# Performance work log

Measured on AMD Instinct MI355X. Metric: run time of the kernel, lower is better.

Reference implementation:

```python
import jax, jax.numpy as jnp
import numpy as np
import math

B, W, V, D, H, L = 64, 255, 16389, 512, 8, 8
S = W + 1          # window + cls token
NLOC = V - 5       # n_locations
CLS = V - 1        # cls_index = 16388
DH = D // H
FF = 4 * D


def _pe(seq_len, d):
    # Faithful to the quirky PositionalEmbedding: for even col c, sin(pos/10000**(2c/d));
    # for odd col c (= i+1), cos(pos/10000**(2c/d)) since it uses 2*(i+1)/d.
    pos = np.arange(seq_len, dtype=np.float32)[:, None]
    c = np.arange(d, dtype=np.float32)[None, :]
    ang = pos / (10000.0 ** (2.0 * c / d))
    pe = np.where(np.arange(d)[None, :] % 2 == 0, np.sin(ang), np.cos(ang))
    return jnp.asarray(pe, jnp.float32)

PE = _pe(S, D)


def _ln(x, s, b):
    m = x.mean(-1, keepdims=True)
    v = ((x - m) ** 2).mean(-1, keepdims=True)
    return (x - m) * jax.lax.rsqrt(v + 1e-5) * s + b


def setup_inputs() -> dict:
    key = jax.random.key(0)
    ks = jax.random.split(key, 8)
    sd = 0.02
    return {
        "x": jax.random.randint(ks[0], (B, W), 0, NLOC),
        "emb": jax.random.normal(ks[1], (V, D), jnp.float32) * sd,
        "qkv_w": jax.random.normal(ks[2], (L, D, 3 * D), jnp.float32) * sd,
        "qkv_b": jnp.zeros((L, 3 * D), jnp.float32),
        "out_w": jax.random.normal(ks[3], (L, D, D), jnp.float32) * sd,
        "out_b": jnp.zeros((L, D), jnp.float32),
        "ln1_s": jnp.ones((L, D), jnp.float32),
        "ln1_b": jnp.zeros((L, D), jnp.float32),
        "ln2_s": jnp.ones((L, D), jnp.float32),
        "ln2_b": jnp.zeros((L, D), jnp.float32),
        "ff1_w": jax.random.normal(ks[4], (L, D, FF), jnp.float32) * sd,
        "ff1_b": jnp.zeros((L, FF), jnp.float32),
        "ff2_w": jax.random.normal(ks[5], (L, FF, D), jnp.float32) * sd,
        "ff2_b": jnp.zeros((L, D), jnp.float32),
        "fn_s": jnp.ones((D,), jnp.float32),
        "fn_b": jnp.zeros((D,), jnp.float32),
        "head_w": jax.random.normal(ks[6], (D, V), jnp.float32) * sd,
    }


def _forward(x, emb, qkv_w, qkv_b, out_w, out_b, ln1_s, ln1_b, ln2_s, ln2_b,
             ff1_w, ff1_b, ff2_w, ff2_b, fn_s, fn_b, head_w):
    b = x.shape[0]
    xc = jnp.concatenate([x, jnp.full((b, 1), CLS, x.dtype)], axis=1)  # [B,S]
    h = emb[xc] + PE[None, :, :]

    def layer(h, p):
        qw, qb, ow, ob, l1s, l1b, l2s, l2b, w1, b1, w2, b2 = p
        x2 = _ln(h, l1s, l1b)
        qkv = x2 @ qw + qb                       # [B,S,3D]
        q, k, v = jnp.split(qkv, 3, axis=-1)
        sh = lambda t: t.reshape(b, S, H, DH).transpose(0, 2, 1, 3)  # [B,H,S,DH]
        q, k, v = sh(q), sh(k), sh(v)
        scores = jnp.einsum('bhqd,bhkd->bhqk', q, k) / math.sqrt(DH)
        attn = jax.nn.softmax(scores, axis=-1)
        o = jnp.einsum('bhqk,bhkd->bhqd', attn, v)
        o = o.transpose(0, 2, 1, 3).reshape(b, S, D)
        h = h + (o @ ow + ob)
        x2 = _ln(h, l2s, l2b)
        h = h + (jax.nn.relu(x2 @ w1 + b1) @ w2 + b2)
        return h, None

    h, _ = jax.lax.scan(layer, h, (qkv_w, qkv_b, out_w, out_b, ln1_s, ln1_b,
                                   ln2_s, ln2_b, ff1_w, ff1_b, ff2_w, ff2_b))
    h = _ln(h, fn_s, fn_b)
    # original projects every position then slices [:, -1, :NLOC]; projecting
    # only the last position with the first NLOC columns is identical math.
    return h[:, -1, :] @ head_w[:, :NLOC]        # [B, NLOC]


def reference(x, emb, qkv_w, qkv_b, out_w, out_b, ln1_s, ln1_b, ln2_s, ln2_b,
              ff1_w, ff1_b, ff2_w, ff2_b, fn_s, fn_b, head_w):
    return _forward(x, emb, qkv_w, qkv_b, out_w, out_b, ln1_s, ln1_b, ln2_s,
                    ln2_b, ff1_w, ff1_b, ff2_w, ff2_b, fn_s, fn_b, head_w)
```

## Files before the change

kernel.cpp:

```cpp
#include <hip/hip_runtime.h>
#include <hip/hip_bf16.h>
#include <math.h>

#define B_    64
#define W_    255
#define S_    256
#define V_    16389
#define NLOC_ 16384
#define CLS_  16388
#define D_    512
#define H_    8
#define DH_   64
#define FF_   2048
#define L_    8
#define NTOK  (B_ * S_)

typedef __attribute__((ext_vector_type(4)))  float f32x4;
typedef __attribute__((ext_vector_type(16))) float f32x16;
typedef __attribute__((ext_vector_type(8)))  short s16x8;

__device__ inline unsigned short f2b(float f) {
  union { float f; unsigned u; } v; v.f = f;
  unsigned r = v.u + 0x7fff + ((v.u >> 16) & 1);
  return (unsigned short)(r >> 16);
}
__device__ inline void gl_lds16(const void* g, void* l) {
  __builtin_amdgcn_global_load_lds((const __attribute__((address_space(1))) unsigned int*)g,
                                   (__attribute__((address_space(3))) unsigned int*)l, 16, 0, 0);
}
__device__ inline size_t tiled_off(int row, int k, int Kb) {
  return ((size_t)(row >> 7) * Kb + (k >> 5)) * 4096 +
         ((((k >> 3) & 3) * 128 + (row & 127)) * 8) + (k & 7);
}

__global__ __launch_bounds__(256) void embed_kernel(const int* __restrict__ x,
                                                    const float* __restrict__ emb,
                                                    float* __restrict__ h) {
  const int tok = blockIdx.x;
  const int bb = tok >> 8, ss = tok & 255;
  const int idx = (ss < W_) ? x[bb * W_ + ss] : CLS_;
  const float* e = emb + (size_t)idx * D_;
  float* hp = h + (size_t)tok * D_;
  #pragma unroll
  for (int r = 0; r < 2; ++r) {
    int d = threadIdx.x + r * 256;
    float ex = exp2f(-(float)d * (13.287712379549449f / 256.0f));
    float ang = (float)ss * ex;
    float pe = (d & 1) ? cosf(ang) : sinf(ang);
    hp[d] = e[d] + pe;
  }
}

template<bool TILED>
__global__ __launch_bounds__(256) void ln_kernel(const float* __restrict__ in,
                                                 unsigned short* __restrict__ out,
                                                 const float* __restrict__ sc,
                                                 const float* __restrict__ bi) {
  const int wave = threadIdx.x >> 6;
  const int tok = blockIdx.x * 4 + wave;
  const int lane = threadIdx.x & 63;
  const float* xp = in + (size_t)tok * D_;
  float4 a = *(const float4*)(xp + lane * 4);
  float4 b = *(const float4*)(xp + 256 + lane * 4);
  float sum = a.x + a.y + a.z + a.w + b.x + b.y + b.z + b.w;
  #pragma unroll
  for (int off = 32; off; off >>= 1) sum += __shfl_xor(sum, off);
  const float mean = sum * (1.0f / D_);
  float d0 = a.x - mean, d1 = a.y - mean, d2 = a.z - mean, d3 = a.w - mean;
  float e0 = b.x - mean, e1 = b.y - mean, e2 = b.z - mean, e3 = b.w - mean;
  float ss = d0*d0 + d1*d1 + d2*d2 + d3*d3 + e0*e0 + e1*e1 + e2*e2 + e3*e3;
  #pragma unroll
  for (int off = 32; off; off >>= 1) ss += __shfl_xor(ss, off);
  const float inv = rsqrtf(ss * (1.0f / D_) + 1e-5f);
  float4 s0 = *(const float4*)(sc + lane * 4);
  float4 s1 = *(const float4*)(sc + 256 + lane * 4);
  float4 b0 = *(const float4*)(bi + lane * 4);
  float4 b1 = *(const float4*)(bi + 256 + lane * 4);
  unsigned short o[8];
  o[0] = f2b(d0 * inv * s0.x + b0.x); o[1] = f2b(d1 * inv * s0.y + b0.y);
  o[2] = f2b(d2 * inv * s0.z + b0.z); o[3] = f2b(d3 * inv * s0.w + b0.w);
  o[4] = f2b(e0 * inv * s1.x + b1.x); o[5] = f2b(e1 * inv * s1.y + b1.y);
  o[6] = f2b(e2 * inv * s1.z + b1.z); o[7] = f2b(e3 * inv * s1.w + b1.w);
  if (!TILED) {
    unsigned short* yp = out + (size_t)tok * D_;
    *(ushort4*)(yp + lane * 4)       = *(const ushort4*)&o[0];
    *(ushort4*)(yp + 256 + lane * 4) = *(const ushort4*)&o[4];
  } else {
    __shared__ unsigned short Xs[4][512];
    *(ushort4*)&Xs[wave][lane * 4]       = *(const ushort4*)&o[0];
    *(ushort4*)&Xs[wave][256 + lane * 4] = *(const ushort4*)&o[4];
    __syncthreads();
    const int c = threadIdx.x >> 2, tr = threadIdx.x & 3;
    const int tok0 = blockIdx.x * 4;
    const int rb = tok0 >> 7, r = (tok0 & 127) + tr;
    s16x8 v = *(const s16x8*)&Xs[tr][c * 8];
    *(s16x8*)(out + ((size_t)rb * 16 + (c >> 2)) * 4096 + ((c & 3) * 128 + r) * 8) = v;
  }
}

__global__ __launch_bounds__(256) void wconv_kernel(const float* __restrict__ W,
                                                    unsigned short* __restrict__ Wt,
                                                    int ldn, int Kb,
                                                    long in_stride, long out_stride) {
  const float* Wl = W + (size_t)blockIdx.z * in_stride;
  unsigned short* Wo = Wt + (size_t)blockIdx.z * out_stride +
                       ((size_t)blockIdx.x * Kb + blockIdx.y) * 4096;
  const int k0 = blockIdx.y * 32, n0 = blockIdx.x * 128;
  #pragma unroll
  for (int qq = 0; qq < 2; ++qq) {
    int q = qq * 256 + threadIdx.x;
    int c = q >> 7, r = q & 127;
    unsigned short o[8];
    #pragma unroll
    for (int j = 0; j < 8; ++j)
      o[j] = f2b(Wl[(size_t)(k0 + c * 8 + j) * ldn + n0 + r]);
    *(s16x8*)(Wo + (size_t)q * 8) = *(const s16x8*)o;
  }
}

template<bool BIAS, bool RELU, bool RES, bool OUTBF, bool ATILED, bool OUTTILED>
__global__ __launch_bounds__(256) void mfma_gemm(
    const unsigned short* __restrict__ A, long lda,
    const unsigned short* __restrict__ Bt,
    const float* __restrict__ bias,
    float* __restrict__ Cres,
    unsigned short* __restrict__ Cbf,
    int M, int N, int K, int ldc, int kbo) {
  __shared__ __align__(16) unsigned char smem[16384];
  unsigned short* As = (unsigned short*)smem;
  unsigned short* Bs = As + 128 * 32;
  const int tid = threadIdx.x;
  const int w = tid >> 6, lane = tid & 63;
  const int wm = w >> 1, wn = w & 1;
  int bx, by;
  {
    int nx = gridDim.x, ny = gridDim.y;
    int id = blockIdx.y * nx + blockIdx.x;
    if ((ny & 7) == 0) {
      int xcd = id & 7, k = id >> 3, band = ny >> 3;
      int kr = k / nx;
      by = xcd * band + kr;
      bx = k - kr * nx;
    } else { bx = blockIdx.x; by = blockIdx.y; }
  }
  const int row0 = by * 128, col0 = bx * 128;
  const int KbB = K >> 5;
  f32x16 acc[2][2] = {};
  const int fl = lane & 31, fg2 = lane >> 5;
  const int sc8 = w * 8;
  for (int k0 = 0; k0 < K; k0 += 32) {
    if (ATILED) {
      const unsigned short* at = A + ((size_t)(row0 >> 7) * lda + (k0 >> 5)) * 4096;
      gl_lds16(at + (size_t)tid * 8, As + (size_t)tid * 8);
      gl_lds16(at + (size_t)(256 + tid) * 8, As + (size_t)(256 + tid) * 8);
    } else {
      #pragma unroll
      for (int i = 0; i < 2; ++i) {
        int r = i * 64 + lane;
        int ar = row0 + r; if (ar >= M) ar = M - 1;
        gl_lds16(A + (size_t)ar * lda + k0 + sc8, As + (w * 2 + i) * 512);
      }
    }
    {
      const unsigned short* bt = Bt + ((size_t)(col0 >> 7) * KbB + (k0 >> 5)) * 4096;
      gl_lds16(bt + (size_t)tid * 8, Bs + (size_t)tid * 8);
      gl_lds16(bt + (size_t)(256 + tid) * 8, Bs + (size_t)(256 + tid) * 8);
    }
    __syncthreads();
    #pragma unroll
    for (int ks = 0; ks < 2; ++ks) {
      s16x8 af[2], bf2[2];
      #pragma unroll
      for (int mi = 0; mi < 2; ++mi)
        af[mi] = *(const s16x8*)&As[((ks * 2 + fg2) * 128 + wm * 64 + mi * 32 + fl) * 8];
      #pragma unroll
      for (int ni = 0; ni < 2; ++ni)
        bf2[ni] = *(const s16x8*)&Bs[((ks * 2 + fg2) * 128 + wn * 64 + ni * 32 + fl) * 8];
      #pragma unroll
      for (int mi = 0; mi < 2; ++mi)
        #pragma unroll
        for (int ni = 0; ni < 2; ++ni)
          acc[mi][ni] = __builtin_amdgcn_mfma_f32_32x32x16_bf16(af[mi], bf2[ni], acc[mi][ni], 0, 0, 0);
    }
    __syncthreads();
  }
  if (OUTTILED) {
    unsigned short* Cs = (unsigned short*)smem;
    #pragma unroll
    for (int half = 0; half < 2; ++half) {
      __syncthreads();
      if (wm == half) {
        #pragma unroll
        for (int mi = 0; mi < 2; ++mi)
          #pragma unroll
          for (int ni = 0; ni < 2; ++ni) {
            int col = wn * 64 + ni * 32 + fl;
            float bv = BIAS ? bias[col0 + col] : 0.0f;
            #pragma unroll
            for (int rg = 0; rg < 16; ++rg) {
              int rl = mi * 32 + (rg & 3) + 8 * (rg >> 2) + 4 * fg2;
              float v = acc[mi][ni][rg] + bv;
              if (RELU) v = fmaxf(v, 0.0f);
              Cs[((col >> 3) * 64 + rl) * 8 + (col & 7)] = f2b(v);
            }
          }
      }
      __syncthreads();
      #pragma unroll
      for (int i = 0; i < 4; ++i) {
        int vt = i * 256 + tid;
        int c = vt >> 6, r = vt & 63;
        int cg = (col0 >> 3) + c;
        s16x8 v = *(const s16x8*)&Cs[(size_t)vt * 8];
        *(s16x8*)(Cbf + ((size_t)(row0 >> 7) * kbo + (cg >> 2)) * 4096 +
                  ((cg & 3) * 128 + half * 64 + r) * 8) = v;
      }
    }
  } else if (OUTBF) {
    unsigned short* Cs = (unsigned short*)smem;
    #pragma unroll
    for (int half = 0; half < 2; ++half) {
      __syncthreads();
      if (wm == half) {
        #pragma unroll
        for (int mi = 0; mi < 2; ++mi)
          #pragma unroll
          for (int ni = 0; ni < 2; ++ni) {
            int col = wn * 64 + ni * 32 + fl;
            float bv = BIAS ? bias[col0 + col] : 0.0f;
            #pragma unroll
            for (int rg = 0; rg < 16; ++rg) {
              int rl = mi * 32 + (rg & 3) + 8 * (rg >> 2) + 4 * fg2;
              float v = acc[mi][ni][rg] + bv;
              if (RELU) v = fmaxf(v, 0.0f);
              Cs[rl * 128 + col] = f2b(v);
            }
          }
      }
      __syncthreads();
      #pragma unroll
      for (int i = 0; i < 4; ++i) {
        int chunk = i * 256 + tid;
        int row = chunk >> 4, cc = chunk & 15;
        int grow = row0 + half * 64 + row;
        *(s16x8*)(Cbf + (size_t)grow * ldc + col0 + cc * 8) =
            *(const s16x8*)&Cs[row * 128 + cc * 8];
      }
    }
  } else {
    float* Csf = (float*)smem;
    #pragma unroll
    for (int q = 0; q < 4; ++q) {
      __syncthreads();
      if (wm == (q >> 1)) {
        const int mi = q & 1;
        #pragma unroll
        for (int ni = 0; ni < 2; ++ni) {
          int col = wn * 64 + ni * 32 + fl;
          float bv = BIAS ? bias[col0 + col] : 0.0f;
          #pragma unroll
          for (int rg = 0; rg < 16; ++rg) {
            int rl = (rg & 3) + 8 * (rg >> 2) + 4 * fg2;
            float v = acc[mi][ni][rg] + bv;
            if (RELU) v = fmaxf(v, 0.0f);
            Csf[rl * 128 + col] = v;
          }
        }
      }
      __syncthreads();
      #pragma unroll
      for (int i = 0; i < 4; ++i) {
        int chunk = i * 256 + tid;
        int row = chunk >> 5, cc = chunk & 31;
        int grow = row0 + q * 32 + row;
        if (grow < M) {
          float4 v = *(const float4*)&Csf[row * 128 + cc * 4];
          float* gp = Cres + (size_t)grow * ldc + col0 + cc * 4;
          if (RES) {
            float4 hv = *(const float4*)gp;
            v.x += hv.x; v.y += hv.y; v.z += hv.z; v.w += hv.w;
          }
          *(float4*)gp = v;
        }
      }
    }
  }
}

__global__ __launch_bounds__(256) void vt_kernel(const unsigned short* __restrict__ qkvb,
                                                 unsigned short* __restrict__ vtg) {
  const int bh = blockIdx.x;
  const int jt = blockIdx.y;
  const int bb = bh >> 3, hh = bh & 7;
  __shared__ unsigned short t[64][72];
  const int r = threadIdx.x >> 2;
  const int c = (threadIdx.x & 3) * 16;
  const unsigned short* src = qkvb + (size_t)(bb * 256 + jt * 64 + r) * 1536 + 1024 + hh * 64 + c;
  *(s16x8*)&t[r][c]     = *(const s16x8*)src;
  *(s16x8*)&t[r][c + 8] = *(const s16x8*)(src + 8);
  __syncthreads();
  unsigned short tmp[16];
  #pragma unroll
  for (int i = 0; i < 16; ++i) tmp[i] = t[c + i][r];
  unsigned short* dst = vtg + ((size_t)bh * 64 + r) * 256 + jt * 64 + c;
  *(s16x8*)dst       = *(const s16x8*)&tmp[0];
  *(s16x8*)(dst + 8) = *(const s16x8*)&tmp[8];
}

__global__ __launch_bounds__(256) void attn_mfma(const unsigned short* __restrict__ qkvb,
                                                 const unsigned short* __restrict__ vtg,
                                                 unsigned short* __restrict__ obuf) {
  const int bh = blockIdx.x;
  const int bb = bh >> 3, hh = bh & 7;
  const int tid = threadIdx.x, w = tid >> 6, lane = tid & 63;
  __shared__ unsigned short Pl[4][16][264];
  const int fr = lane & 15, fg = lane >> 4;
  const unsigned short* qbase = qkvb + (size_t)bb * 256 * 1536 + hh * 64;
  const unsigned short* kbase = qbase + 512;
  const unsigned short* vb = vtg + (size_t)bh * 64 * 256;

  for (int s = w; s < 16; s += 4) {
    const int q0 = s * 16;
    f32x4 sacc[16] = {};
    s16x8 aq[2];
    #pragma unroll
    for (int kk = 0; kk < 2; ++kk)
      aq[kk] = *(const s16x8*)(qbase + (size_t)(q0 + fr) * 1536 + kk * 32 + fg * 8);
    #pragma unroll
    for (int ni = 0; ni < 16; ++ni) {
      #pragma unroll
      for (int kk = 0; kk < 2; ++kk) {
        s16x8 bk = *(const s16x8*)(kbase + (size_t)(ni * 16 + fr) * 1536 + kk * 32 + fg * 8);
        sacc[ni] = __builtin_amdgcn_mfma_f32_16x16x32_bf16(aq[kk], bk, sacc[ni], 0, 0, 0);
      }
    }
    #pragma unroll
    for (int rr = 0; rr < 4; ++rr) {
      float mx = -1e30f;
      #pragma unroll
      for (int ni = 0; ni < 16; ++ni) mx = fmaxf(mx, sacc[ni][rr]);
      #pragma unroll
      for (int off = 1; off <= 8; off <<= 1) mx = fmaxf(mx, __shfl_xor(mx, off));
      float sum = 0.0f;
      #pragma unroll
      for (int ni = 0; ni < 16; ++ni) {
        float e = __expf((sacc[ni][rr] - mx) * 0.125f);
        sacc[ni][rr] = e; sum += e;
      }
      #pragma unroll
      for (int off = 1; off <= 8; off <<= 1) sum += __shfl_xor(sum, off);
      float inv = 1.0f / sum;
      #pragma unroll
      for (int ni = 0; ni < 16; ++ni) sacc[ni][rr] *= inv;
    }
    #pragma unroll
    for (int ni = 0; ni < 16; ++ni)
      #pragma unroll
      for (int rr = 0; rr < 4; ++rr)
        Pl[w][fg * 4 + rr][ni * 16 + fr] = f2b(sacc[ni][rr]);
    f32x4 oacc[4] = {};
    #pragma unroll
    for (int kk = 0; kk < 8; ++kk) {
      s16x8 ap = *(const s16x8*)&Pl[w][fr][kk * 32 + fg * 8];
      #pragma unroll
      for (int ni = 0; ni < 4; ++ni) {
        s16x8 bv = *(const s16x8*)(vb + (size_t)(ni * 16 + fr) * 256 + kk * 32 + fg * 8);
        oacc[ni] = __builtin_amdgcn_mfma_f32_16x16x32_bf16(ap, bv, oacc[ni], 0, 0, 0);
      }
    }
    #pragma unroll
    for (int ni = 0; ni < 4; ++ni)
      #pragma unroll
      for (int rr = 0; rr < 4; ++rr) {
        int row = bb * 256 + q0 + fg * 4 + rr;
        int k = hh * 64 + ni * 16 + fr;
        obuf[tiled_off(row, k, 16)] = f2b(oacc[ni][rr]);
      }
  }
}

extern "C" void kernel_launch(void* const* d_in, const int* in_sizes, int n_in,
                              void* d_out, int out_size, void* d_ws, size_t ws_size,
                              hipStream_t stream) {
  const int*   x      = (const int*)  d_in[0];
  const float* emb    = (const float*)d_in[1];
  const float* qkv_w  = (const float*)d_in[2];
  const float* qkv_b  = (const float*)d_in[3];
  const float* out_w  = (const float*)d_in[4];
  const float* out_b  = (const float*)d_in[5];
  const float* ln1_s  = (const float*)d_in[6];
  const float* ln1_b  = (const float*)d_in[7];
  const float* ln2_s  = (const float*)d_in[8];
  const float* ln2_b  = (const float*)d_in[9];
  const float* ff1_w  = (const float*)d_in[10];
  const float* ff1_b  = (const float*)d_in[11];
  const float* ff2_w  = (const float*)d_in[12];
  const float* ff2_b  = (const float*)d_in[13];
  const float* fn_s   = (const float*)d_in[14];
  const float* fn_b   = (const float*)d_in[15];
  const float* head_w = (const float*)d_in[16];
  float* out = (float*)d_out;

  char* p = (char*)d_ws;
  float* h = (float*)p;                      p += (size_t)NTOK * D_ * 4;
  unsigned short* x2b = (unsigned short*)p;  p += (size_t)NTOK * D_ * 2;
  unsigned short* qkvb = (unsigned short*)p; p += (size_t)NTOK * 3 * D_ * 2;
  unsigned short* vtg = (unsigned short*)p;  p += (size_t)B_ * H_ * DH_ * S_ * 2;
  unsigned short* obuf = (unsigned short*)p; p += (size_t)NTOK * D_ * 2;
  unsigned short* wt_qkv = (unsigned short*)p; p += (size_t)L_ * D_ * 3 * D_ * 2;
  unsigned short* wt_out = (unsigned short*)p; p += (size_t)L_ * D_ * D_ * 2;
  unsigned short* wt_ff1 = (unsigned short*)p; p += (size_t)L_ * D_ * FF_ * 2;
  unsigned short* wt_ff2 = (unsigned short*)p; p += (size_t)FF_ * D_ * L_ * 2;
  unsigned short* wth = (unsigned short*)p;    p += (size_t)NLOC_ * D_ * 2;
  unsigned short* ffmid = qkvb;

  embed_kernel<<<NTOK, 256, 0, stream>>>(x, emb, h);
  wconv_kernel<<<dim3(3 * D_ / 128, D_ / 32, L_), 256, 0, stream>>>(
      qkv_w, wt_qkv, 3 * D_, D_ / 32, (long)D_ * 3 * D_, (long)D_ * 3 * D_);
  wconv_kernel<<<dim3(D_ / 128, D_ / 32, L_), 256, 0, stream>>>(
      out_w, wt_out, D_, D_ / 32, (long)D_ * D_, (long)D_ * D_);
  wconv_kernel<<<dim3(FF_ / 128, D_ / 32, L_), 256, 0, stream>>>(
      ff1_w, wt_ff1, FF_, D_ / 32, (long)D_ * FF_, (long)D_ * FF_);
  wconv_kernel<<<dim3(D_ / 128, FF_ / 32, L_), 256, 0, stream>>>(
      ff2_w, wt_ff2, D_, FF_ / 32, (long)FF_ * D_, (long)FF_ * D_);
  wconv_kernel<<<dim3(NLOC_ / 128, D_ / 32, 1), 256, 0, stream>>>(
      head_w, wth, V_, D_ / 32, 0, 0);

  for (int l = 0; l < L_; ++l) {
    ln_kernel<true><<<NTOK / 4, 256, 0, stream>>>(h, x2b, ln1_s + l * D_, ln1_b + l * D_);
    mfma_gemm<true, false, false, true, true, false><<<dim3(3 * D_ / 128, NTOK / 128), 256, 0, stream>>>(
        x2b, 16, wt_qkv + (size_t)l * D_ * 3 * D_, qkv_b + (size_t)l * 3 * D_, nullptr, qkvb,
        NTOK, 3 * D_, D_, 3 * D_, 0);
    vt_kernel<<<dim3(B_ * H_, 4), 256, 0, stream>>>(qkvb, vtg);
    attn_mfma<<<B_ * H_, 256, 0, stream>>>(qkvb, vtg, obuf);
    mfma_gemm<true, false, true, false, true, false><<<dim3(D_ / 128, NTOK / 128), 256, 0, stream>>>(
        obuf, 16, wt_out + (size_t)l * D_ * D_, out_b + (size_t)l * D_, h, nullptr,
        NTOK, D_, D_, D_, 0);
    ln_kernel<true><<<NTOK / 4, 256, 0, stream>>>(h, x2b, ln2_s + l * D_, ln2_b + l * D_);
    mfma_gemm<true, true, false, true, true, true><<<dim3(FF_ / 128, NTOK / 128), 256, 0, stream>>>(
        x2b, 16, wt_ff1 + (size_t)l * D_ * FF_, ff1_b + (size_t)l * FF_, nullptr, ffmid,
        NTOK, FF_, D_, FF_, 64);
    mfma_gemm<true, false, true, false, true, false><<<dim3(D_ / 128, NTOK / 128), 256, 0, stream>>>(
        ffmid, 64, wt_ff2 + (size_t)l * FF_ * D_, ff2_b + (size_t)l * D_, h, nullptr,
        NTOK, D_, FF_, D_, 0);
  }
  ln_kernel<false><<<NTOK / 4, 256, 0, stream>>>(h, x2b, fn_s, fn_b);
  mfma_gemm<false, false, false, false, false, false><<<dim3(NLOC_ / 128, 1), 256, 0, stream>>>(
      x2b + (size_t)(S_ - 1) * D_, (long)S_ * D_, wth, nullptr, out, nullptr,
      B_, NLOC_, D_, NLOC_, 0);
}
```

Measured before the change: 2.296 ms.

## Enlarge layer GEMM tiles to 256 rows with templated column width

Replaces the 128x128 tiled GEMM used for QKV, out-projection, FF1 and FF2 with a larger-tile kernel: 256 rows by 256 columns for QKV/FF1 and 256x128 for the D-wide outputs, with each wave holding 4xNI MFMA accumulators. The aim is more arithmetic per LDS byte and fewer A/B tile reloads from global memory. The epilogues are rewritten for padded LDS staging in four row rounds. The head GEMM is split into its own simple kernel. Tradeoffs: more accumulator registers and a larger LDS footprint lower occupancy, and the grid gets smaller (for example 1536/256 x 64 blocks).

```diff
diff --git a/kernel.cpp b/kernel.cpp
--- a/kernel.cpp
+++ b/kernel.cpp
@@ -118,17 +118,18 @@
   }
 }
 
-template<bool BIAS, bool RELU, bool RES, bool OUTBF, bool ATILED, bool OUTTILED>
-__global__ __launch_bounds__(256) void mfma_gemm(
-    const unsigned short* __restrict__ A, long lda,
+template<int NI, bool BIAS, bool RELU, bool RES, bool OUTBF, bool OUTTILED>
+__global__ __launch_bounds__(256) void mfma_gemm_big(
+    const unsigned short* __restrict__ A, long KbA,
     const unsigned short* __restrict__ Bt,
     const float* __restrict__ bias,
     float* __restrict__ Cres,
     unsigned short* __restrict__ Cbf,
     int M, int N, int K, int ldc, int kbo) {
-  __shared__ __align__(16) unsigned char smem[16384];
+  __shared__ __align__(16) unsigned char smem[33792];
   unsigned short* As = (unsigned short*)smem;
-  unsigned short* Bs = As + 128 * 32;
+  unsigned short* Bs = As + 8192;
+  constexpr int NB = NI / 2;
   const int tid = threadIdx.x;
   const int w = tid >> 6, lane = tid & 63;
   const int wm = w >> 1, wn = w & 1;
@@ -143,23 +144,153 @@
       bx = k - kr * nx;
     } else { bx = blockIdx.x; by = blockIdx.y; }
   }
-  const int row0 = by * 128, col0 = bx * 128;
+  const int row0 = by * 256, col0 = bx * (NI * 64);
+  const int KbB = K >> 5;
+  f32x16 acc[4][NI] = {};
+  const int fl = lane & 31, fg2 = lane >> 5;
+  for (int k0 = 0; k0 < K; k0 += 32) {
+    const int kb = k0 >> 5;
+    #pragma unroll
+    for (int s = 0; s < 2; ++s) {
+      const unsigned short* at = A + ((size_t)((row0 >> 7) + s) * KbA + kb) * 4096;
+      gl_lds16(at + (size_t)tid * 8, As + s * 4096 + (size_t)tid * 8);
+      gl_lds16(at + (size_t)(256 + tid) * 8, As + s * 4096 + (size_t)(256 + tid) * 8);
+    }
+    #pragma unroll
+    for (int s = 0; s < NB; ++s) {
+      const unsigned short* bt = Bt + ((size_t)((col0 >> 7) + s) * KbB + kb) * 4096;
+      gl_lds16(bt + (size_t)tid * 8, Bs + s * 4096 + (size_t)tid * 8);
+      gl_lds16(bt + (size_t)(256 + tid) * 8, Bs + s * 4096 + (size_t)(256 + tid) * 8);
+    }
+    __syncthreads();
+    #pragma unroll
+    for (int ks = 0; ks < 2; ++ks) {
+      s16x8 af[4], bf2[NI];
+      #pragma unroll
+      for (int mi = 0; mi < 4; ++mi)
+        af[mi] = *(const s16x8*)&As[wm * 4096 + ((ks * 2 + fg2) * 128 + mi * 32 + fl) * 8];
+      #pragma unroll
+      for (int ni = 0; ni < NI; ++ni) {
+        int cl = wn * (NI * 32) + ni * 32 + fl;
+        bf2[ni] = *(const s16x8*)&Bs[(cl >> 7) * 4096 + ((ks * 2 + fg2) * 128 + (cl & 127)) * 8];
+      }
+      #pragma unroll
+      for (int mi = 0; mi < 4; ++mi)
+        #pragma unroll
+        for (int ni = 0; ni < NI; ++ni)
+          acc[mi][ni] = __builtin_amdgcn_mfma_f32_32x32x16_bf16(af[mi], bf2[ni], acc[mi][ni], 0, 0, 0);
+    }
+    __syncthreads();
+  }
+  constexpr int C = NI * 64;
+  if (OUTBF || OUTTILED) {
+    unsigned short* Cs = (unsigned short*)smem;
+    #pragma unroll
+    for (int rnd = 0; rnd < 4; ++rnd) {
+      __syncthreads();
+      if (wm == (rnd >> 1)) {
+        #pragma unroll
+        for (int miL = 0; miL < 2; ++miL) {
+          int mi = (rnd & 1) * 2 + miL;
+          #pragma unroll
+          for (int ni = 0; ni < NI; ++ni) {
+            int col = wn * (NI * 32) + ni * 32 + fl;
+            float bv = BIAS ? bias[col0 + col] : 0.0f;
+            #pragma unroll
+            for (int rg = 0; rg < 16; ++rg) {
+              int rl = miL * 32 + (rg & 3) + 8 * (rg >> 2) + 4 * fg2;
+              float v = acc[mi][ni][rg] + bv;
+              if (RELU) v = fmaxf(v, 0.0f);
+              Cs[rl * 264 + col] = f2b(v);
+            }
+          }
+        }
+      }
+      __syncthreads();
+      if (OUTTILED) {
+        #pragma unroll
+        for (int i = 0; i < C / 32; ++i) {
+          int q = i * 256 + tid;
+          int g = q >> 6, rl = q & 63;
+          int grow = row0 + rnd * 64 + rl;
+          int cg = (col0 >> 3) + g;
+          *(s16x8*)(Cbf + ((size_t)(grow >> 7) * kbo + (cg >> 2)) * 4096 +
+                    ((cg & 3) * 128 + (grow & 127)) * 8) =
+              *(const s16x8*)&Cs[rl * 264 + g * 8];
+        }
+      } else {
+        #pragma unroll
+        for (int i = 0; i < C / 32; ++i) {
+          int q = i * 256 + tid;
+          int row = q / (C / 8), cc = q & (C / 8 - 1);
+          *(s16x8*)(Cbf + (size_t)(row0 + rnd * 64 + row) * ldc + col0 + cc * 8) =
+              *(const s16x8*)&Cs[row * 264 + cc * 8];
+        }
+      }
+    }
+  } else {
+    float* Csf = (float*)smem;
+    #pragma unroll
+    for (int rnd = 0; rnd < 4; ++rnd) {
+      __syncthreads();
+      if (wm == (rnd >> 1)) {
+        #pragma unroll
+        for (int miL = 0; miL < 2; ++miL) {
+          int mi = (rnd & 1) * 2 + miL;
+          #pragma unroll
+          for (int ni = 0; ni < NI; ++ni) {
+            int col = wn * (NI * 32) + ni * 32 + fl;
+            float bv = BIAS ? bias[col0 + col] : 0.0f;
+            #pragma unroll
+            for (int rg = 0; rg < 16; ++rg) {
+              int rl = miL * 32 + (rg & 3) + 8 * (rg >> 2) + 4 * fg2;
+              float v = acc[mi][ni][rg] + bv;
+              if (RELU) v = fmaxf(v, 0.0f);
+              Csf[rl * 132 + col] = v;
+            }
+          }
+        }
+      }
+      __syncthreads();
+      #pragma unroll
+      for (int i = 0; i < 8; ++i) {
+        int q = i * 256 + tid;
+        int rl = q >> 5, cc = q & 31;
+        int grow = row0 + rnd * 64 + rl;
+        float4 v = *(const float4*)&Csf[rl * 132 + cc * 4];
+        float* gp = Cres + (size_t)grow * ldc + col0 + cc * 4;
+        if (RES) {
+          float4 hv = *(const float4*)gp;
+          v.x += hv.x; v.y += hv.y; v.z += hv.z; v.w += hv.w;
+        }
+        *(float4*)gp = v;
+      }
+    }
+  }
+}
+
+__global__ __launch_bounds__(256) void head_gemm(
+    const unsigned short* __restrict__ A, long lda,
+    const unsigned short* __restrict__ Bt,
+    float* __restrict__ Cres,
+    int M, int N, int K, int ldc) {
+  __shared__ __align__(16) unsigned char smem[16384];
+  unsigned short* As = (unsigned short*)smem;
+  unsigned short* Bs = As + 128 * 32;
+  const int tid = threadIdx.x;
+  const int w = tid >> 6, lane = tid & 63;
+  const int wm = w >> 1, wn = w & 1;
+  const int row0 = blockIdx.y * 128, col0 = blockIdx.x * 128;
   const int KbB = K >> 5;
   f32x16 acc[2][2] = {};
   const int fl = lane & 31, fg2 = lane >> 5;
   const int sc8 = w * 8;
   for (int k0 = 0; k0 < K; k0 += 32) {
-    if (ATILED) {
-      const unsigned short* at = A + ((size_t)(row0 >> 7) * lda + (k0 >> 5)) * 4096;
-      gl_lds16(at + (size_t)tid * 8, As + (size_t)tid * 8);
-      gl_lds16(at + (size_t)(256 + tid) * 8, As + (size_t)(256 + tid) * 8);
-    } else {
-      #pragma unroll
-      for (int i = 0; i < 2; ++i) {
-        int r = i * 64 + lane;
-        int ar = row0 + r; if (ar >= M) ar = M - 1;
-        gl_lds16(A + (size_t)ar * lda + k0 + sc8, As + (w * 2 + i) * 512);
-      }
+    #pragma unroll
+    for (int i = 0; i < 2; ++i) {
+      int r = i * 64 + lane;
+      int ar = row0 + r; if (ar >= M) ar = M - 1;
+      gl_lds16(A + (size_t)ar * lda + k0 + sc8, As + (w * 2 + i) * 512);
     }
     {
       const unsigned short* bt = Bt + ((size_t)(col0 >> 7) * KbB + (k0 >> 5)) * 4096;
@@ -184,104 +315,31 @@
     }
     __syncthreads();
   }
-  if (OUTTILED) {
-    unsigned short* Cs = (unsigned short*)smem;
-    #pragma unroll
-    for (int half = 0; half < 2; ++half) {
-      __syncthreads();
-      if (wm == half) {
-        #pragma unroll
-        for (int mi = 0; mi < 2; ++mi)
-          #pragma unroll
-          for (int ni = 0; ni < 2; ++ni) {
-            int col = wn * 64 + ni * 32 + fl;
-            float bv = BIAS ? bias[col0 + col] : 0.0f;
-            #pragma unroll
-            for (int rg = 0; rg < 16; ++rg) {
-              int rl = mi * 32 + (rg & 3) + 8 * (rg >> 2) + 4 * fg2;
-              float v = acc[mi][ni][rg] + bv;
-              if (RELU) v = fmaxf(v, 0.0f);
-              Cs[((col >> 3) * 64 + rl) * 8 + (col & 7)] = f2b(v);
-            }
-          }
-      }
-      __syncthreads();
-      #pragma unroll
-      for (int i = 0; i < 4; ++i) {
-        int vt = i * 256 + tid;
-        int c = vt >> 6, r = vt & 63;
-        int cg = (col0 >> 3) + c;
-        s16x8 v = *(const s16x8*)&Cs[(size_t)vt * 8];
-        *(s16x8*)(Cbf + ((size_t)(row0 >> 7) * kbo + (cg >> 2)) * 4096 +
-                  ((cg & 3) * 128 + half * 64 + r) * 8) = v;
-      }
-    }
-  } else if (OUTBF) {
-    unsigned short* Cs = (unsigned short*)smem;
-    #pragma unroll
-    for (int half = 0; half < 2; ++half) {
-      __syncthreads();
-      if (wm == half) {
-        #pragma unroll
-        for (int mi = 0; mi < 2; ++mi)
-          #pragma unroll
-          for (int ni = 0; ni < 2; ++ni) {
-            int col = wn * 64 + ni * 32 + fl;
-            float bv = BIAS ? bias[col0 + col] : 0.0f;
-            #pragma unroll
-            for (int rg = 0; rg < 16; ++rg) {
-              int rl = mi * 32 + (rg & 3) + 8 * (rg >> 2) + 4 * fg2;
-              float v = acc[mi][ni][rg] + bv;
-              if (RELU) v = fmaxf(v, 0.0f);
-              Cs[rl * 128 + col] = f2b(v);
-            }
-          }
-      }
-      __syncthreads();
-      #pragma unroll
-      for (int i = 0; i < 4; ++i) {
-        int chunk = i * 256 + tid;
-        int row = chunk >> 4, cc = chunk & 15;
-        int grow = row0 + half * 64 + row;
-        *(s16x8*)(Cbf + (size_t)grow * ldc + col0 + cc * 8) =
-            *(const s16x8*)&Cs[row * 128 + cc * 8];
-      }
-    }
-  } else {
-    float* Csf = (float*)smem;
-    #pragma unroll
-    for (int q = 0; q < 4; ++q) {
-      __syncthreads();
-      if (wm == (q >> 1)) {
-        const int mi = q & 1;
-        #pragma unroll
-        for (int ni = 0; ni < 2; ++ni) {
-          int col = wn * 64 + ni * 32 + fl;
-          float bv = BIAS ? bias[col0 + col] : 0.0f;
-          #pragma unroll
-          for (int rg = 0; rg < 16; ++rg) {
-            int rl = (rg & 3) + 8 * (rg >> 2) + 4 * fg2;
-            float v = acc[mi][ni][rg] + bv;
-            if (RELU) v = fmaxf(v, 0.0f);
-            Csf[rl * 128 + col] = v;
-          }
+  float* Csf = (float*)smem;
+  #pragma unroll
+  for (int q = 0; q < 4; ++q) {
+    __syncthreads();
+    if (wm == (q >> 1)) {
+      const int mi = q & 1;
+      #pragma unroll
+      for (int ni = 0; ni < 2; ++ni) {
+        int col = wn * 64 + ni * 32 + fl;
+        #pragma unroll
+        for (int rg = 0; rg < 16; ++rg) {
+          int rl = (rg & 3) + 8 * (rg >> 2) + 4 * fg2;
+          Csf[rl * 128 + col] = acc[mi][ni][rg];
         }
       }
-      __syncthreads();
-      #pragma unroll
-      for (int i = 0; i < 4; ++i) {
-        int chunk = i * 256 + tid;
-        int row = chunk >> 5, cc = chunk & 31;
-        int grow = row0 + q * 32 + row;
-        if (grow < M) {
-          float4 v = *(const float4*)&Csf[row * 128 + cc * 4];
-          float* gp = Cres + (size_t)grow * ldc + col0 + cc * 4;
-          if (RES) {
-            float4 hv = *(const float4*)gp;
-            v.x += hv.x; v.y += hv.y; v.z += hv.z; v.w += hv.w;
-          }
-          *(float4*)gp = v;
-        }
+    }
+    __syncthreads();
+    #pragma unroll
+    for (int i = 0; i < 4; ++i) {
+      int chunk = i * 256 + tid;
+      int row = chunk >> 5, cc = chunk & 31;
+      int grow = row0 + q * 32 + row;
+      if (grow < M) {
+        float4 v = *(const float4*)&Csf[row * 128 + cc * 4];
+        *(float4*)(Cres + (size_t)grow * ldc + col0 + cc * 4) = v;
       }
     }
   }
@@ -428,24 +486,23 @@
 
   for (int l = 0; l < L_; ++l) {
     ln_kernel<true><<<NTOK / 4, 256, 0, stream>>>(h, x2b, ln1_s + l * D_, ln1_b + l * D_);
-    mfma_gemm<true, false, false, true, true, false><<<dim3(3 * D_ / 128, NTOK / 128), 256, 0, stream>>>(
+    mfma_gemm_big<4, true, false, false, true, false><<<dim3(3 * D_ / 256, NTOK / 256), 256, 0, stream>>>(
         x2b, 16, wt_qkv + (size_t)l * D_ * 3 * D_, qkv_b + (size_t)l * 3 * D_, nullptr, qkvb,
         NTOK, 3 * D_, D_, 3 * D_, 0);
     vt_kernel<<<dim3(B_ * H_, 4), 256, 0, stream>>>(qkvb, vtg);
     attn_mfma<<<B_ * H_, 256, 0, stream>>>(qkvb, vtg, obuf);
-    mfma_gemm<true, false, true, false, true, false><<<dim3(D_ / 128, NTOK / 128), 256, 0, stream>>>(
+    mfma_gemm_big<2, true, false, true, false, false><<<dim3(D_ / 128, NTOK / 256), 256, 0, stream>>>(
         obuf, 16, wt_out + (size_t)l * D_ * D_, out_b + (size_t)l * D_, h, nullptr,
         NTOK, D_, D_, D_, 0);
     ln_kernel<true><<<NTOK / 4, 256, 0, stream>>>(h, x2b, ln2_s + l * D_, ln2_b + l * D_);
-    mfma_gemm<true, true, false, true, true, true><<<dim3(FF_ / 128, NTOK / 128), 256, 0, stream>>>(
+    mfma_gemm_big<4, true, true, false, false, true><<<dim3(FF_ / 256, NTOK / 256), 256, 0, stream>>>(
         x2b, 16, wt_ff1 + (size_t)l * D_ * FF_, ff1_b + (size_t)l * FF_, nullptr, ffmid,
         NTOK, FF_, D_, FF_, 64);
-    mfma_gemm<true, false, true, false, true, false><<<dim3(D_ / 128, NTOK / 128), 256, 0, stream>>>(
+    mfma_gemm_big<2, true, false, true, false, false><<<dim3(D_ / 128, NTOK / 256), 256, 0, stream>>>(
         ffmid, 64, wt_ff2 + (size_t)l * FF_ * D_, ff2_b + (size_t)l * D_, h, nullptr,
         NTOK, D_, FF_, D_, 0);
   }
   ln_kernel<false><<<NTOK / 4, 256, 0, stream>>>(h, x2b, fn_s, fn_b);
-  mfma_gemm<false, false, false, false, false, false><<<dim3(NLOC_ / 128, 1), 256, 0, stream>>>(
-      x2b + (size_t)(S_ - 1) * D_, (long)S_ * D_, wth, nullptr, out, nullptr,
-      B_, NLOC_, D_, NLOC_, 0);
-}
+  head_gemm<<<dim3(NLOC_ / 128, 1), 256, 0, stream>>>(
+      x2b + (size_t)(S_ - 1) * D_, (long)S_ * D_, wth, out, B_, NLOC_, D_, NLOC_);
+}
```

Result: slower. 2.763 ms (+20.3%).
